# Optimization experiments

Hardware: AMD Instinct MI355X
Metric: run time of the kernel (lower is better)

## Reference

```python
import jax, jax.numpy as jnp
import numpy as np

DECAY = 0.9


def setup_inputs() -> dict:
    key = jax.random.key(0)
    k1, k2 = jax.random.split(key)
    x = jax.random.normal(k1, (8, 2048, 512), dtype=jnp.float32)
    key_embed = jax.random.normal(k2, (8, 2048, 64), dtype=jnp.float32)
    return {"x": x, "key_embed": key_embed, "key_optim": 1}


def reference(x, key_embed, key_optim):
    # key_embed: [h, c, d]
    h, c, d = key_embed.shape
    b, t, _ = x.shape
    x = x.astype(jnp.float32)
    # 'b t (h d) -> h b t d'
    xh = x.reshape(b, t, h, d).transpose(2, 0, 1, 3)  # [h, b, t, d]
    flat = xh.reshape(h, b * t, d)                     # [h, n, d]

    # nearest codebook entry: argmax(-cdist) == argmin of squared distance
    x_sq = jnp.sum(flat * flat, axis=-1, keepdims=True)           # [h, n, 1]
    e_sq = jnp.sum(key_embed * key_embed, axis=-1)[:, None, :]    # [h, 1, c]
    dots = jnp.einsum('hnd,hcd->hnc', flat, key_embed)            # [h, n, c]
    d2 = x_sq - 2.0 * dots + e_sq
    ind = jnp.argmin(d2, axis=-1)                                 # [h, n]
    emb_ind = ind.reshape(h, b, t)                                # [h, b, t]

    # gather quantized vectors: [h, b, t, d]
    head_idx = jnp.arange(h)[:, None, None]
    quantized = key_embed[head_idx, emb_ind]

    # EMA codebook update: key_embed.lerp_(emb_sum, decay)
    emb_sum = jnp.zeros_like(key_embed).at[jnp.arange(h)[:, None], ind].add(flat)
    if key_optim:
        new_key_embed = key_embed + DECAY * (emb_sum - key_embed)
    else:
        new_key_embed = key_embed

    # 'h b t d -> b t (h d)'
    quant_out = quantized.transpose(1, 2, 0, 3).reshape(b, t, h * d)
    # 'h b n -> b n h'
    emb_ind_out = emb_ind.transpose(1, 2, 0)
    return (quant_out, emb_ind_out, new_key_embed)
```

## Files before the change

### kernel.cpp

```cpp
#include <hip/hip_runtime.h>
#include <float.h>

#define H   8
#define C   2048
#define D   64
#define NPH 16384
#define HD  512
#define DECAYF 0.9f
#define DELTA 3.0f
#define CAP 64
#define VB  256

typedef __attribute__((ext_vector_type(8))) short short8v;
typedef __attribute__((ext_vector_type(4))) float f32x4;

__device__ inline unsigned short f32_to_bf16_rne(float f) {
    unsigned int x = __float_as_uint(f);
    return (unsigned short)((x + 0x7FFFu + ((x >> 16) & 1u)) >> 16);
}

__global__ __launch_bounds__(256) void vq_prep_kernel(const float* __restrict__ ke,
                                                      unsigned short* __restrict__ keb2,
                                                      float* __restrict__ esq,
                                                      unsigned int* __restrict__ counts) {
    const int row = blockIdx.x * 256 + threadIdx.x;
    const int c   = row & 15;
    const int ch  = (row >> 4) & 127;
    const int h   = row >> 11;
    const float* e = ke + (size_t)row * D;
    unsigned short* kb = keb2 + ((size_t)h * C * D) + (size_t)ch * 1024;
#pragma unroll
    for (int kf = 0; kf < 2; ++kf)
#pragma unroll
        for (int g = 0; g < 4; ++g) {
            float4 v0 = ((const float4*)e)[kf * 8 + g * 2];
            float4 v1 = ((const float4*)e)[kf * 8 + g * 2 + 1];
            short8v o;
            o[0] = (short)f32_to_bf16_rne(v0.x); o[1] = (short)f32_to_bf16_rne(v0.y);
            o[2] = (short)f32_to_bf16_rne(v0.z); o[3] = (short)f32_to_bf16_rne(v0.w);
            o[4] = (short)f32_to_bf16_rne(v1.x); o[5] = (short)f32_to_bf16_rne(v1.y);
            o[6] = (short)f32_to_bf16_rne(v1.z); o[7] = (short)f32_to_bf16_rne(v1.w);
            *(short8v*)(kb + kf * 512 + (g * 16 + c) * 8) = o;
        }
    float s = 0.f;
#pragma unroll
    for (int d = 0; d < D; ++d) s = fmaf(e[d], e[d], s);
    esq[row] = s;
    counts[row] = 0u;
}

__global__ __launch_bounds__(256, 2)
void vq_main_kernel(const float* __restrict__ x,
                    const unsigned short* __restrict__ keb2,
                    const float* __restrict__ ke,
                    const float* __restrict__ esq,
                    float* __restrict__ outq,
                    float* __restrict__ outi,
                    unsigned short* __restrict__ indw,
                    unsigned int* __restrict__ counts) {
    __shared__ int            ccnt[VB];
    __shared__ unsigned short cand[VB][CAP];
    __shared__ int            sidx[VB];

    const int tid  = threadIdx.x;
    const int lane = tid & 63;
    const int w    = __builtin_amdgcn_readfirstlane(tid >> 6);
    const int h    = blockIdx.x & 7;
    const int n0   = (blockIdx.x >> 3) * VB;

    const unsigned short* keb2h = keb2 + (size_t)h * C * D;
    const float* keh  = ke  + (size_t)h * C * D;
    const float* esqh = esq + (size_t)h * C;

    ccnt[tid] = 0;
    __syncthreads();

    const int col = lane & 15;
    const int kg  = (lane >> 4) * 8;

    short8v afr[4][2];
#pragma unroll
    for (int vt = 0; vt < 4; ++vt) {
        const float* xp = x + (size_t)(n0 + w * 64 + vt * 16 + col) * HD
                            + (size_t)h * D + kg;
#pragma unroll
        for (int kf = 0; kf < 2; ++kf) {
            float4 u0 = *(const float4*)(xp + kf * 32);
            float4 u1 = *(const float4*)(xp + kf * 32 + 4);
            short8v a;
            a[0] = (short)f32_to_bf16_rne(u0.x); a[1] = (short)f32_to_bf16_rne(u0.y);
            a[2] = (short)f32_to_bf16_rne(u0.z); a[3] = (short)f32_to_bf16_rne(u0.w);
            a[4] = (short)f32_to_bf16_rne(u1.x); a[5] = (short)f32_to_bf16_rne(u1.y);
            a[6] = (short)f32_to_bf16_rne(u1.z); a[7] = (short)f32_to_bf16_rne(u1.w);
            afr[vt][kf] = a;
        }
    }

    float amin[16];
#pragma unroll
    for (int s = 0; s < 16; ++s) amin[s] = FLT_MAX;

#define LOADB2(CH, B0, B1, EQ)                                                 \
    {                                                                          \
        const short8v* kb = (const short8v*)(keb2h + (size_t)(CH) * 1024);     \
        B0 = kb[lane];                                                         \
        B1 = kb[64 + lane];                                                    \
        EQ = esqh[((CH) << 4) + col];                                          \
    }

#define MFMA4(C0V, C1V, A0, A1, A2, A3)                                        \
    {                                                                          \
        A0 = (f32x4){0.f, 0.f, 0.f, 0.f};                                      \
        A1 = (f32x4){0.f, 0.f, 0.f, 0.f};                                      \
        A2 = (f32x4){0.f, 0.f, 0.f, 0.f};                                      \
        A3 = (f32x4){0.f, 0.f, 0.f, 0.f};                                      \
        A0 = __builtin_amdgcn_mfma_f32_16x16x32_bf16(afr[0][0], C0V, A0, 0, 0, 0); \
        A1 = __builtin_amdgcn_mfma_f32_16x16x32_bf16(afr[1][0], C0V, A1, 0, 0, 0); \
        A2 = __builtin_amdgcn_mfma_f32_16x16x32_bf16(afr[2][0], C0V, A2, 0, 0, 0); \
        A3 = __builtin_amdgcn_mfma_f32_16x16x32_bf16(afr[3][0], C0V, A3, 0, 0, 0); \
        A0 = __builtin_amdgcn_mfma_f32_16x16x32_bf16(afr[0][1], C1V, A0, 0, 0, 0); \
        A1 = __builtin_amdgcn_mfma_f32_16x16x32_bf16(afr[1][1], C1V, A1, 0, 0, 0); \
        A2 = __builtin_amdgcn_mfma_f32_16x16x32_bf16(afr[2][1], C1V, A2, 0, 0, 0); \
        A3 = __builtin_amdgcn_mfma_f32_16x16x32_bf16(afr[3][1], C1V, A3, 0, 0, 0); \
    }

#define EPI1(A0, A1, A2, A3, QV)                                               \
    {                                                                          \
        _Pragma("unroll")                                                      \
        for (int r = 0; r < 4; ++r) {                                          \
            amin[0 + r]  = fminf(amin[0 + r],  fmaf(-2.f, A0[r], QV));         \
            amin[4 + r]  = fminf(amin[4 + r],  fmaf(-2.f, A1[r], QV));         \
            amin[8 + r]  = fminf(amin[8 + r],  fmaf(-2.f, A2[r], QV));         \
            amin[12 + r] = fminf(amin[12 + r], fmaf(-2.f, A3[r], QV));         \
        }                                                                      \
    }

#define EPI2(A0, A1, A2, A3, QV, CB)                                           \
    {                                                                          \
        _Pragma("unroll")                                                      \
        for (int vt = 0; vt < 4; ++vt) {                                       \
            const f32x4 aa = (vt == 0) ? A0 : (vt == 1) ? A1 : (vt == 2) ? A2 : A3; \
            _Pragma("unroll")                                                  \
            for (int r = 0; r < 4; ++r) {                                      \
                float sc = fmaf(-2.f, aa[r], QV);                              \
                if (sc <= amin[vt * 4 + r] + DELTA) {                          \
                    const int vec = w * 64 + vt * 16 + ((lane >> 4) << 2) + r; \
                    int pos = atomicAdd(&ccnt[vec], 1);                        \
                    if (pos < CAP) cand[vec][pos] = (unsigned short)((CB) + col); \
                }                                                              \
            }                                                                  \
        }                                                                      \
    }

    {
        short8v s0a, s0b, s1a, s1b, s2a, s2b, s3a, s3b;
        float   q0, q1, q2, q3;
        LOADB2(0, s0a, s0b, q0);
        LOADB2(1, s1a, s1b, q1);
        LOADB2(2, s2a, s2b, q2);
        LOADB2(3, s3a, s3b, q3);
        f32x4 xA0, xA1, xA2, xA3, yA0, yA1, yA2, yA3;
#pragma unroll 1
        for (int g = 0; g < 32; ++g) {
            {
                short8v c0 = s0a, c1 = s0b; float qa = q0;
                short8v d0 = s1a, d1 = s1b; float qb = q1;
                LOADB2((4 * g + 4) & 127, s0a, s0b, q0);
                LOADB2((4 * g + 5) & 127, s1a, s1b, q1);
                MFMA4(c0, c1, xA0, xA1, xA2, xA3);
                MFMA4(d0, d1, yA0, yA1, yA2, yA3);
                EPI1(xA0, xA1, xA2, xA3, qa);
                EPI1(yA0, yA1, yA2, yA3, qb);
            }
            {
                short8v c0 = s2a, c1 = s2b; float qa = q2;
                short8v d0 = s3a, d1 = s3b; float qb = q3;
                LOADB2((4 * g + 6) & 127, s2a, s2b, q2);
                LOADB2((4 * g + 7) & 127, s3a, s3b, q3);
                MFMA4(c0, c1, xA0, xA1, xA2, xA3);
                MFMA4(d0, d1, yA0, yA1, yA2, yA3);
                EPI1(xA0, xA1, xA2, xA3, qa);
                EPI1(yA0, yA1, yA2, yA3, qb);
            }
        }
    }

#pragma unroll
    for (int s = 0; s < 16; ++s) {
        float v = amin[s];
        v = fminf(v, __shfl_xor(v, 1));
        v = fminf(v, __shfl_xor(v, 2));
        v = fminf(v, __shfl_xor(v, 4));
        v = fminf(v, __shfl_xor(v, 8));
        amin[s] = v;
    }

    {
        short8v s0a, s0b, s1a, s1b, s2a, s2b, s3a, s3b;
        float   q0, q1, q2, q3;
        LOADB2(0, s0a, s0b, q0);
        LOADB2(1, s1a, s1b, q1);
        LOADB2(2, s2a, s2b, q2);
        LOADB2(3, s3a, s3b, q3);
        f32x4 xA0, xA1, xA2, xA3, yA0, yA1, yA2, yA3;
#pragma unroll 1
        for (int g = 0; g < 32; ++g) {
            {
                short8v c0 = s0a, c1 = s0b; float qa = q0;
                short8v d0 = s1a, d1 = s1b; float qb = q1;
                LOADB2((4 * g + 4) & 127, s0a, s0b, q0);
                LOADB2((4 * g + 5) & 127, s1a, s1b, q1);
                MFMA4(c0, c1, xA0, xA1, xA2, xA3);
                MFMA4(d0, d1, yA0, yA1, yA2, yA3);
                EPI2(xA0, xA1, xA2, xA3, qa, (4 * g + 0) << 4);
                EPI2(yA0, yA1, yA2, yA3, qb, (4 * g + 1) << 4);
            }
            {
                short8v c0 = s2a, c1 = s2b; float qa = q2;
                short8v d0 = s3a, d1 = s3b; float qb = q3;
                LOADB2((4 * g + 6) & 127, s2a, s2b, q2);
                LOADB2((4 * g + 7) & 127, s3a, s3b, q3);
                MFMA4(c0, c1, xA0, xA1, xA2, xA3);
                MFMA4(d0, d1, yA0, yA1, yA2, yA3);
                EPI2(xA0, xA1, xA2, xA3, qa, (4 * g + 2) << 4);
                EPI2(yA0, yA1, yA2, yA3, qb, (4 * g + 3) << 4);
            }
        }
    }
    __syncthreads();

    {
        const float4* xr = (const float4*)(x + (size_t)(n0 + tid) * HD + (size_t)h * D);
        const int nc = ccnt[tid];
        float bb = FLT_MAX;
        int   bi = 0x7fffffff;
        if (nc <= CAP) {
            for (int i = 0; i < nc; ++i) {
                const int code = cand[tid][i];
                const float4* er = (const float4*)(keh + (size_t)code * D);
                float s = 0.f;
#pragma unroll 4
                for (int kq = 0; kq < 16; ++kq) {
                    float4 a4 = xr[kq]; float4 e4 = er[kq];
                    s = fmaf(a4.x, e4.x, s); s = fmaf(a4.y, e4.y, s);
                    s = fmaf(a4.z, e4.z, s); s = fmaf(a4.w, e4.w, s);
                }
                float sc = fmaf(-2.f, s, esqh[code]);
                if (sc < bb || (sc == bb && code < bi)) { bb = sc; bi = code; }
            }
        } else {
            for (int code = 0; code < C; ++code) {
                const float4* er = (const float4*)(keh + (size_t)code * D);
                float s = 0.f;
#pragma unroll 4
                for (int kq = 0; kq < 16; ++kq) {
                    float4 a4 = xr[kq]; float4 e4 = er[kq];
                    s = fmaf(a4.x, e4.x, s); s = fmaf(a4.y, e4.y, s);
                    s = fmaf(a4.z, e4.z, s); s = fmaf(a4.w, e4.w, s);
                }
                float sc = fmaf(-2.f, s, esqh[code]);
                if (sc < bb) { bb = sc; bi = code; }
            }
        }
        sidx[tid] = bi;
        outi[(size_t)(n0 + tid) * H + h] = (float)bi;
        indw[((size_t)h << 14) + n0 + tid] = (unsigned short)bi;
        atomicAdd(&counts[(h << 11) + bi], 1u);
    }
    __syncthreads();

#pragma unroll
    for (int ii = 0; ii < 2; ++ii) {
        const int v  = ii * 128 + (tid >> 1);
        const int db = (tid & 1) * 32;
        const int ci = sidx[v];
        const float* ev = keh + (size_t)ci * D + db;
        float* qo = outq + (size_t)(n0 + v) * HD + (size_t)h * D + db;
#pragma unroll
        for (int i = 0; i < 8; ++i)
            ((float4*)qo)[i] = ((const float4*)ev)[i];
    }
}

__global__ __launch_bounds__(256) void vq_scan_kernel(const unsigned int* __restrict__ counts,
                                                      unsigned int* __restrict__ off,
                                                      unsigned int* __restrict__ cur) {
    __shared__ unsigned int sa[C], sb[C];
    const int h   = blockIdx.x;
    const int tid = threadIdx.x;
#pragma unroll
    for (int j = 0; j < 8; ++j) sa[j * 256 + tid] = counts[(h << 11) + j * 256 + tid];
    __syncthreads();
    unsigned int* src = sa;
    unsigned int* dst = sb;
    for (int s = 1; s < C; s <<= 1) {
#pragma unroll
        for (int j = 0; j < 8; ++j) {
            const int c = j * 256 + tid;
            unsigned int v = src[c];
            if (c >= s) v += src[c - s];
            dst[c] = v;
        }
        __syncthreads();
        unsigned int* t = src; src = dst; dst = t;
    }
#pragma unroll
    for (int j = 0; j < 8; ++j) {
        const int c = j * 256 + tid;
        const unsigned int e = c ? src[c - 1] : 0u;
        off[(h << 11) + c] = e;
        cur[(h << 11) + c] = e;
    }
}

__global__ __launch_bounds__(256) void vq_scatter_kernel(const unsigned short* __restrict__ ind,
                                                         unsigned int* __restrict__ cur,
                                                         unsigned int* __restrict__ perm) {
    const int g = blockIdx.x * 256 + threadIdx.x;
    const int h = g >> 14;
    const int n = g & 16383;
    const int c = ind[g];
    const unsigned int pos = atomicAdd(&cur[(h << 11) + c], 1u);
    perm[((size_t)h << 14) + pos] = (unsigned int)n;
}

__global__ __launch_bounds__(256) void vq_reduce_kernel(const float* __restrict__ x,
                                                        const float* __restrict__ ke,
                                                        const unsigned int* __restrict__ perm,
                                                        const unsigned int* __restrict__ counts,
                                                        const unsigned int* __restrict__ off,
                                                        const int* __restrict__ ko,
                                                        float* __restrict__ outk) {
    __shared__ double sred[3][64];
    const int tid  = threadIdx.x;
    const int lane = tid & 63;
    const int w    = tid >> 6;
    const int pair = blockIdx.x;
    const int h    = pair >> 11;

    const unsigned int cnt = counts[pair];
    const unsigned int o   = off[pair];
    const unsigned int* pl = perm + ((size_t)h << 14) + o;
    const float* xh = x + (size_t)h * D;

    double a0 = 0.0, a1 = 0.0, a2 = 0.0, a3 = 0.0;
    unsigned int i = (unsigned int)w;
    for (; i + 12 < cnt; i += 16) {
        const unsigned int v0 = pl[i], v1 = pl[i + 4], v2 = pl[i + 8], v3 = pl[i + 12];
        a0 += (double)xh[(size_t)v0 * HD + lane];
        a1 += (double)xh[(size_t)v1 * HD + lane];
        a2 += (double)xh[(size_t)v2 * HD + lane];
        a3 += (double)xh[(size_t)v3 * HD + lane];
    }
    for (; i < cnt; i += 4)
        a0 += (double)xh[(size_t)pl[i] * HD + lane];
    const double part = ((a0 + a1) + a2) + a3;

    if (w) sred[w - 1][lane] = part;
    __syncthreads();
    if (w == 0) {
        const double acc = ((part + sred[0][lane]) + sred[1][lane]) + sred[2][lane];
        const float esum = (float)acc;
        const float kv   = ke[(size_t)pair * D + lane];
        const float ov   = ko[0] ? (kv + DECAYF * (esum - kv)) : kv;
        outk[(size_t)pair * D + lane] = ov;
    }
}

extern "C" void kernel_launch(void* const* d_in, const int* in_sizes, int n_in,
                              void* d_out, int out_size, void* d_ws, size_t ws_size,
                              hipStream_t stream) {
    const float* x  = (const float*)d_in[0];
    const float* ke = (const float*)d_in[1];
    const int*   ko = (const int*)d_in[2];

    float* out  = (float*)d_out;
    float* outq = out;
    float* outi = out + (size_t)H * NPH * D;
    float* outk = outi + (size_t)NPH * H;

    float*          esq    = (float*)d_ws;
    unsigned short* keb2   = (unsigned short*)(esq + H * C);
    unsigned short* indw   = keb2 + (size_t)H * C * D;
    unsigned int*   counts = (unsigned int*)(indw + (size_t)H * NPH);
    unsigned int*   offv   = counts + H * C;
    unsigned int*   curv   = offv + H * C;
    unsigned int*   perm   = curv + H * C;

    vq_prep_kernel<<<(H * C) / 256, 256, 0, stream>>>(ke, keb2, esq, counts);
    vq_main_kernel<<<512, 256, 0, stream>>>(x, keb2, ke, esq, outq, outi, indw, counts);
    vq_scan_kernel<<<H, 256, 0, stream>>>(counts, offv, curv);
    vq_scatter_kernel<<<512, 256, 0, stream>>>(indw, curv, perm);
    vq_reduce_kernel<<<H * C, 256, 0, stream>>>(x, ke, perm, counts, offv, ko, outk);
}
```

Baseline: 194.5 us.

## Fuse two-pass approximate argmin into single pass with running min threshold

After: 286.8 us. +47.5%, slower.

```diff
diff --git a/kernel.cpp b/kernel.cpp
--- a/kernel.cpp
+++ b/kernel.cpp
@@ -135,97 +135,98 @@
         }                                                                      \
     }
 
-#define EPI2(A0, A1, A2, A3, QV, CB)                                           \
+#define EPIC(A0, A1, A2, A3, QV, CB)                                           \
     {                                                                          \
         _Pragma("unroll")                                                      \
         for (int vt = 0; vt < 4; ++vt) {                                       \
             const f32x4 aa = (vt == 0) ? A0 : (vt == 1) ? A1 : (vt == 2) ? A2 : A3; \
             _Pragma("unroll")                                                  \
             for (int r = 0; r < 4; ++r) {                                      \
+                const int s = vt * 4 + r;                                      \
                 float sc = fmaf(-2.f, aa[r], QV);                              \
-                if (sc <= amin[vt * 4 + r] + DELTA) {                          \
+                if (sc <= amin[s] + DELTA) {                                   \
                     const int vec = w * 64 + vt * 16 + ((lane >> 4) << 2) + r; \
                     int pos = atomicAdd(&ccnt[vec], 1);                        \
                     if (pos < CAP) cand[vec][pos] = (unsigned short)((CB) + col); \
                 }                                                              \
+                if (sc < amin[s]) amin[s] = sc;                                \
             }                                                                  \
         }                                                                      \
     }
 
-    {
-        short8v s0a, s0b, s1a, s1b, s2a, s2b, s3a, s3b;
-        float   q0, q1, q2, q3;
-        LOADB2(0, s0a, s0b, q0);
-        LOADB2(1, s1a, s1b, q1);
-        LOADB2(2, s2a, s2b, q2);
-        LOADB2(3, s3a, s3b, q3);
-        f32x4 xA0, xA1, xA2, xA3, yA0, yA1, yA2, yA3;
+#define SYNC_AMIN                                                              \
+    {                                                                          \
+        _Pragma("unroll")                                                      \
+        for (int s = 0; s < 16; ++s) {                                         \
+            float v = amin[s];                                                 \
+            v = fminf(v, __shfl_xor(v, 1));                                    \
+            v = fminf(v, __shfl_xor(v, 2));                                    \
+            v = fminf(v, __shfl_xor(v, 4));                                    \
+            v = fminf(v, __shfl_xor(v, 8));                                    \
+            amin[s] = v;                                                       \
+        }                                                                      \
+    }
+
+    short8v s0a, s0b, s1a, s1b, s2a, s2b, s3a, s3b;
+    float   q0, q1, q2, q3;
+    f32x4   xA0, xA1, xA2, xA3, yA0, yA1, yA2, yA3;
+    LOADB2(0, s0a, s0b, q0);
+    LOADB2(1, s1a, s1b, q1);
+    LOADB2(2, s2a, s2b, q2);
+    LOADB2(3, s3a, s3b, q3);
+
 #pragma unroll 1
-        for (int g = 0; g < 32; ++g) {
-            {
-                short8v c0 = s0a, c1 = s0b; float qa = q0;
-                short8v d0 = s1a, d1 = s1b; float qb = q1;
-                LOADB2((4 * g + 4) & 127, s0a, s0b, q0);
-                LOADB2((4 * g + 5) & 127, s1a, s1b, q1);
-                MFMA4(c0, c1, xA0, xA1, xA2, xA3);
-                MFMA4(d0, d1, yA0, yA1, yA2, yA3);
-                EPI1(xA0, xA1, xA2, xA3, qa);
-                EPI1(yA0, yA1, yA2, yA3, qb);
-            }
-            {
-                short8v c0 = s2a, c1 = s2b; float qa = q2;
-                short8v d0 = s3a, d1 = s3b; float qb = q3;
-                LOADB2((4 * g + 6) & 127, s2a, s2b, q2);
-                LOADB2((4 * g + 7) & 127, s3a, s3b, q3);
-                MFMA4(c0, c1, xA0, xA1, xA2, xA3);
-                MFMA4(d0, d1, yA0, yA1, yA2, yA3);
-                EPI1(xA0, xA1, xA2, xA3, qa);
-                EPI1(yA0, yA1, yA2, yA3, qb);
-            }
-        }
-    }
-
-#pragma unroll
-    for (int s = 0; s < 16; ++s) {
-        float v = amin[s];
-        v = fminf(v, __shfl_xor(v, 1));
-        v = fminf(v, __shfl_xor(v, 2));
-        v = fminf(v, __shfl_xor(v, 4));
-        v = fminf(v, __shfl_xor(v, 8));
-        amin[s] = v;
-    }
-
-    {
-        short8v s0a, s0b, s1a, s1b, s2a, s2b, s3a, s3b;
-        float   q0, q1, q2, q3;
-        LOADB2(0, s0a, s0b, q0);
-        LOADB2(1, s1a, s1b, q1);
-        LOADB2(2, s2a, s2b, q2);
-        LOADB2(3, s3a, s3b, q3);
-        f32x4 xA0, xA1, xA2, xA3, yA0, yA1, yA2, yA3;
+    for (int g = 0; g < 2; ++g) {
+        {
+            short8v c0 = s0a, c1 = s0b; float qa = q0;
+            short8v d0 = s1a, d1 = s1b; float qb = q1;
+            LOADB2((4 * g + 4) & 127, s0a, s0b, q0);
+            LOADB2((4 * g + 5) & 127, s1a, s1b, q1);
+            MFMA4(c0, c1, xA0, xA1, xA2, xA3);
+            MFMA4(d0, d1, yA0, yA1, yA2, yA3);
+            EPI1(xA0, xA1, xA2, xA3, qa);
+            EPI1(yA0, yA1, yA2, yA3, qb);
+        }
+        {
+            short8v c0 = s2a, c1 = s2b; float qa = q2;
+            short8v d0 = s3a, d1 = s3b; float qb = q3;
+            LOADB2((4 * g + 6) & 127, s2a, s2b, q2);
+            LOADB2((4 * g + 7) & 127, s3a, s3b, q3);
+            MFMA4(c0, c1, xA0, xA1, xA2, xA3);
+            MFMA4(d0, d1, yA0, yA1, yA2, yA3);
+            EPI1(xA0, xA1, xA2, xA3, qa);
+            EPI1(yA0, yA1, yA2, yA3, qb);
+        }
+    }
+    SYNC_AMIN;
+
 #pragma unroll 1
-        for (int g = 0; g < 32; ++g) {
-            {
-                short8v c0 = s0a, c1 = s0b; float qa = q0;
-                short8v d0 = s1a, d1 = s1b; float qb = q1;
-                LOADB2((4 * g + 4) & 127, s0a, s0b, q0);
-                LOADB2((4 * g + 5) & 127, s1a, s1b, q1);
-                MFMA4(c0, c1, xA0, xA1, xA2, xA3);
-                MFMA4(d0, d1, yA0, yA1, yA2, yA3);
-                EPI2(xA0, xA1, xA2, xA3, qa, (4 * g + 0) << 4);
-                EPI2(yA0, yA1, yA2, yA3, qb, (4 * g + 1) << 4);
-            }
-            {
-                short8v c0 = s2a, c1 = s2b; float qa = q2;
-                short8v d0 = s3a, d1 = s3b; float qb = q3;
-                LOADB2((4 * g + 6) & 127, s2a, s2b, q2);
-                LOADB2((4 * g + 7) & 127, s3a, s3b, q3);
-                MFMA4(c0, c1, xA0, xA1, xA2, xA3);
-                MFMA4(d0, d1, yA0, yA1, yA2, yA3);
-                EPI2(xA0, xA1, xA2, xA3, qa, (4 * g + 2) << 4);
-                EPI2(yA0, yA1, yA2, yA3, qb, (4 * g + 3) << 4);
-            }
-        }
+    for (int g = 0; g < 32; ++g) {
+        {
+            const int cbA = ((8 + 4 * g + 0) & 127) << 4;
+            const int cbB = ((8 + 4 * g + 1) & 127) << 4;
+            short8v c0 = s0a, c1 = s0b; float qa = q0;
+            short8v d0 = s1a, d1 = s1b; float qb = q1;
+            LOADB2((4 * g + 12) & 127, s0a, s0b, q0);
+            LOADB2((4 * g + 13) & 127, s1a, s1b, q1);
+            MFMA4(c0, c1, xA0, xA1, xA2, xA3);
+            MFMA4(d0, d1, yA0, yA1, yA2, yA3);
+            EPIC(xA0, xA1, xA2, xA3, qa, cbA);
+            EPIC(yA0, yA1, yA2, yA3, qb, cbB);
+        }
+        {
+            const int cbA = ((8 + 4 * g + 2) & 127) << 4;
+            const int cbB = ((8 + 4 * g + 3) & 127) << 4;
+            short8v c0 = s2a, c1 = s2b; float qa = q2;
+            short8v d0 = s3a, d1 = s3b; float qb = q3;
+            LOADB2((4 * g + 14) & 127, s2a, s2b, q2);
+            LOADB2((4 * g + 15) & 127, s3a, s3b, q3);
+            MFMA4(c0, c1, xA0, xA1, xA2, xA3);
+            MFMA4(d0, d1, yA0, yA1, yA2, yA3);
+            EPIC(xA0, xA1, xA2, xA3, qa, cbA);
+            EPIC(yA0, yA1, yA2, yA3, qb, cbB);
+        }
+        if ((g & 7) == 7) SYNC_AMIN;
     }
     __syncthreads();
 
```
